# Performance work log

Measured on AMD Instinct MI355X. Metric: run time of the kernel, lower is better.

Reference implementation:

```python
import jax, jax.numpy as jnp
import numpy as np

N = 8192          # total nodes (bipartite: first half left, second half right)
E = 65536         # raw edges
D = 256           # emb_dim
H = 8             # heads
HD = D // H       # head_dim = 32
EAD = 2           # edge_attr_dim


def _init(k, shape, fan_in):
    return (jax.random.normal(k, shape, jnp.float32) / np.sqrt(fan_in)).astype(jnp.float32)


def setup_inputs() -> dict:
    key = jax.random.key(0)
    ks = jax.random.split(key, 16)
    x = jax.random.normal(ks[0], (N, D), jnp.float32)
    src = jax.random.randint(ks[1], (E,), 0, N // 2, jnp.int32)
    dst = jax.random.randint(ks[2], (E,), N // 2, N, jnp.int32)
    edge_index = jnp.stack([src, dst])                       # [2, E]
    edge_attr = jax.random.uniform(ks[3], (E, EAD), jnp.float32)
    query_mask = jax.random.randint(ks[4], (E,), 0, 2, jnp.int32).astype(bool)
    return {
        "x": x,
        "edge_index": edge_index,
        "edge_attr": edge_attr,
        "query_mask": query_mask,
        "start_right": N // 2,
        "W_kqv": _init(ks[5], (D, 3 * D), D), "b_kqv": jnp.zeros((3 * D,), jnp.float32),
        "W_edge": _init(ks[6], (EAD, D), EAD), "b_edge": jnp.zeros((D,), jnp.float32),
        "W_att1": _init(ks[7], (3 * HD, HD), 3 * HD), "b_att1": jnp.zeros((HD,), jnp.float32),
        "W_att2": _init(ks[8], (HD, 1), HD), "b_att2": jnp.zeros((1,), jnp.float32),
        "W_out": _init(ks[9], (D, D), D), "b_out": jnp.zeros((D,), jnp.float32),
        "bn_gamma": jnp.ones((D,), jnp.float32), "bn_beta": jnp.zeros((D,), jnp.float32),
    }


def _build_graph(edge_index, query_mask, n):
    """Replicates MetaGNN.forward edge preprocessing (static, int-only)."""
    ei = np.asarray(edge_index)
    qm = np.asarray(query_mask).astype(bool)
    sup = np.where(~qm)[0]                                   # support edges
    # cat([edge_index[:, support], edge_index.flip(0)], dim=1)
    src = np.concatenate([ei[0, sup], ei[1]])
    dst = np.concatenate([ei[1, sup], ei[0]])
    attr_idx = np.concatenate([sup, np.arange(ei.shape[1])])
    # remove_self_loops
    keep = src != dst
    src, dst, attr_idx = src[keep], dst[keep], attr_idx[keep]
    # add_self_loops with fill_value [0, 0]
    loops = np.arange(n)
    src = np.concatenate([src, loops])
    dst = np.concatenate([dst, loops])
    return jnp.asarray(src), jnp.asarray(dst), jnp.asarray(attr_idx)


def _layer(x, src, dst, ea, W_kqv, b_kqv, W_edge, b_edge, W_att1, b_att1,
           W_att2, b_att2, W_out, b_out, bn_gamma, bn_beta):
    n = x.shape[0]
    kqv = x @ W_kqv + b_kqv                                  # [N, 3D]
    q = kqv[dst, :D].reshape(-1, H, HD)                      # x_i (target)
    k = kqv[src, D:2 * D].reshape(-1, H, HD) / np.sqrt(HD)   # x_j (source)
    v = kqv[src, 2 * D:].reshape(-1, H, HD)
    ef = jax.nn.relu((ea @ W_edge + b_edge).reshape(-1, H, HD))
    feat = jnp.concatenate([k, q, ef], axis=-1)              # [E, H, 3*HD]
    hdn = jax.nn.relu(jnp.einsum('ehf,fd->ehd', feat, W_att1) + b_att1)
    logits = (jnp.einsum('ehd,do->eho', hdn, W_att2) + b_att2)[..., 0]  # [E, H]
    # scatter-softmax over destination node segments
    m = jax.ops.segment_max(logits, dst, num_segments=n)
    a = jnp.exp(logits - m[dst])
    s = jax.ops.segment_sum(a, dst, num_segments=n)
    alpha = a / (s[dst] + 1e-16)                             # [E, H]
    msg = (alpha[..., None] * v).reshape(-1, D) @ W_out + b_out
    out = jax.ops.segment_sum(msg, dst, num_segments=n) + x  # aggr='add' + residual
    # BatchNorm1d (training-mode batch statistics, eps=1e-5)
    mu = out.mean(axis=0)
    var = out.var(axis=0)
    return (out - mu) / jnp.sqrt(var + 1e-5) * bn_gamma + bn_beta


def reference(x, edge_index, edge_attr, query_mask, start_right,
              W_kqv, b_kqv, W_edge, b_edge, W_att1, b_att1, W_att2, b_att2,
              W_out, b_out, bn_gamma, bn_beta):
    n = x.shape[0]
    src, dst, attr_idx = _build_graph(edge_index, query_mask, n)
    ea = jnp.concatenate(
        [edge_attr[attr_idx], jnp.zeros((n, edge_attr.shape[1]), edge_attr.dtype)], axis=0)
    return _layer(x, src, dst, ea, W_kqv, b_kqv, W_edge, b_edge,
                  W_att1, b_att1, W_att2, b_att2, W_out, b_out, bn_gamma, bn_beta)
```

## Files before the change

### kernel.cpp

```cpp
#include <hip/hip_runtime.h>

#define N_NODES 8192
#define E_RAW   65536
#define NSLOT   (2*E_RAW + N_NODES)
#define DEGCAP  64

typedef __attribute__((ext_vector_type(8))) short bf16x8;
typedef __attribute__((ext_vector_type(4))) short bf16x4;
typedef __attribute__((ext_vector_type(4))) float f32x4;
typedef unsigned short u16;

__device__ __forceinline__ u16 f2b(float f) {
  unsigned u = __float_as_uint(f);
  u = (u + 0x7FFFu + ((u >> 16) & 1u)) >> 16;
  return (u16)u;
}
__device__ __forceinline__ float b2f(u16 b) {
  return __uint_as_float(((unsigned)b) << 16);
}

__global__ __launch_bounds__(256) void setup_k(
    const float* __restrict__ x, u16* __restrict__ xb,
    const float* __restrict__ W_kqv, const float* __restrict__ b_kqv,
    const float* __restrict__ W_att1, const float* __restrict__ b_att1,
    const float* __restrict__ W_out,
    u16* __restrict__ BcatT, float* __restrict__ biascat,
    u16* __restrict__ wa1t, u16* __restrict__ WoutT,
    const int* __restrict__ ei, const int* __restrict__ qm,
    const float* __restrict__ eattr,
    int* __restrict__ cnt, int* __restrict__ esrc2, float2* __restrict__ ea2)
{
  __shared__ float tile[64][65];
  const float inv_sqrt_hd = 0.17677669529663687f;
  int bx = blockIdx.x, t = threadIdx.x;

  if (bx < 2048) {
    int i = bx * 256 + t;
    float4 v = ((const float4*)x)[i];
    ushort4 o;
    o.x = f2b(v.x); o.y = f2b(v.y); o.z = f2b(v.z); o.w = f2b(v.w);
    ((ushort4*)xb)[i] = o;
    return;
  }
  if (bx < 2836) {
    int c = bx - 2048;
    int i = t;
    if (c < 768) {
      float v;
      if (c < 256) {
        int h = c >> 5, d2 = c & 31;
        float s = 0.f;
        #pragma unroll
        for (int j = 0; j < 32; ++j)
          s += W_kqv[i*768 + 256 + h*32 + j] * W_att1[j*32 + d2];
        v = s * inv_sqrt_hd;
      } else if (c < 512) {
        int c2 = c - 256; int h = c2 >> 5, d2 = c2 & 31;
        float s = 0.f;
        #pragma unroll
        for (int j = 0; j < 32; ++j)
          s += W_kqv[i*768 + h*32 + j] * W_att1[(32+j)*32 + d2];
        v = s;
      } else {
        v = W_kqv[i*768 + c];
      }
      BcatT[(size_t)c * 256 + i] = f2b(v);
      if (i == 0) {
        float bv;
        if (c < 256) {
          int h = c >> 5, d2 = c & 31;
          float s = 0.f;
          for (int j = 0; j < 32; ++j)
            s += b_kqv[256 + h*32 + j] * W_att1[j*32 + d2];
          bv = s * inv_sqrt_hd;
        } else if (c < 512) {
          int c2 = c - 256; int h = c2 >> 5, d2 = c2 & 31;
          float s = 0.f;
          for (int j = 0; j < 32; ++j)
            s += b_kqv[h*32 + j] * W_att1[(32+j)*32 + d2];
          bv = s + b_att1[c2 & 31];
        } else {
          bv = b_kqv[c];
        }
        biascat[c] = bv;
      }
    } else if (c < 772) {
      int idx = (c - 768) * 256 + i;
      int d2 = idx >> 5, j = idx & 31;
      wa1t[idx] = f2b(W_att1[(64 + j) * 32 + d2]);
    } else {
      int b = c - 772;
      int r0 = (b >> 2) * 64, c0 = (b & 3) * 64;
      for (int idx = i; idx < 4096; idx += 256) {
        int r = idx >> 6, cc = idx & 63;
        tile[r][cc] = W_out[(size_t)(r0 + r) * 256 + c0 + cc];
      }
      __syncthreads();
      for (int idx = i; idx < 4096; idx += 256) {
        int cc = idx >> 6, r = idx & 63;
        WoutT[(size_t)(c0 + cc) * 256 + r0 + r] = f2b(tile[r][cc]);
      }
    }
    return;
  }
  int slot = (bx - 2836) * 256 + t;
  if (slot >= NSLOT) return;
  int src, dst; float a0 = 0.f, a1 = 0.f;
  if (slot < E_RAW) {
    if (qm[slot] != 0) return;
    src = ei[slot]; dst = ei[E_RAW + slot];
    a0 = eattr[2*slot]; a1 = eattr[2*slot + 1];
  } else if (slot < 2*E_RAW) {
    int e = slot - E_RAW;
    src = ei[E_RAW + e]; dst = ei[e];
    a0 = eattr[2*e]; a1 = eattr[2*e + 1];
  } else {
    int n = slot - 2*E_RAW;
    src = n; dst = n;
  }
  int pos = atomicAdd(&cnt[dst], 1);
  if (pos < DEGCAP) {
    esrc2[dst*DEGCAP + pos] = src;
    ea2[dst*DEGCAP + pos] = make_float2(a0, a1);
  }
}

__global__ __launch_bounds__(256) void gemm_nf_k(const u16* __restrict__ xb,
                                                 const u16* __restrict__ BcatT,
                                                 const float* __restrict__ biascat,
                                                 u16* __restrict__ nodeF) {
  int t = threadIdx.x, lane = t & 63, wid = t >> 6;
  int r0 = (blockIdx.x * 4 + wid) * 32;
  int c0 = blockIdx.y * 32;
  int lr = lane & 15, lk = (lane >> 4) * 8;
  f32x4 acc00 = {0.f,0.f,0.f,0.f}, acc01 = {0.f,0.f,0.f,0.f};
  f32x4 acc10 = {0.f,0.f,0.f,0.f}, acc11 = {0.f,0.f,0.f,0.f};
  for (int k0 = 0; k0 < 256; k0 += 32) {
    bf16x8 a0 = *(const bf16x8*)&xb[(size_t)(r0 + lr) * 256 + k0 + lk];
    bf16x8 a1 = *(const bf16x8*)&xb[(size_t)(r0 + 16 + lr) * 256 + k0 + lk];
    bf16x8 b0 = *(const bf16x8*)&BcatT[(size_t)(c0 + lr) * 256 + k0 + lk];
    bf16x8 b1 = *(const bf16x8*)&BcatT[(size_t)(c0 + 16 + lr) * 256 + k0 + lk];
    acc00 = __builtin_amdgcn_mfma_f32_16x16x32_bf16(a0, b0, acc00, 0, 0, 0);
    acc01 = __builtin_amdgcn_mfma_f32_16x16x32_bf16(a0, b1, acc01, 0, 0, 0);
    acc10 = __builtin_amdgcn_mfma_f32_16x16x32_bf16(a1, b0, acc10, 0, 0, 0);
    acc11 = __builtin_amdgcn_mfma_f32_16x16x32_bf16(a1, b1, acc11, 0, 0, 0);
  }
  float bias0 = biascat[c0 + lr];
  float bias1 = biascat[c0 + 16 + lr];
  int rbase = r0 + (lane >> 4) * 4;
  #pragma unroll
  for (int r = 0; r < 4; ++r) {
    nodeF[(size_t)(rbase + r) * 768 + c0 + lr]           = f2b(acc00[r] + bias0);
    nodeF[(size_t)(rbase + r) * 768 + c0 + 16 + lr]      = f2b(acc01[r] + bias1);
    nodeF[(size_t)(rbase + 16 + r) * 768 + c0 + lr]      = f2b(acc10[r] + bias0);
    nodeF[(size_t)(rbase + 16 + r) * 768 + c0 + 16 + lr] = f2b(acc11[r] + bias1);
  }
}

__global__ __launch_bounds__(256) void attn_k(
    const int* __restrict__ cnt, const int* __restrict__ esrc2,
    const float2* __restrict__ ea2, const u16* __restrict__ nf,
    const u16* __restrict__ wa1t,
    const float* __restrict__ W_edge, const float* __restrict__ b_edge,
    const float* __restrict__ W_att2,
    u16* __restrict__ aggb)
{
  __shared__ u16   kws[4][2*336];
  __shared__ float lgs[4][DEGCAP*8];

  int t = threadIdx.x, lane = t & 63, wid = t >> 6;
  int n = blockIdx.x * 4 + wid;
  int deg = cnt[n]; if (deg > DEGCAP) deg = DEGCAP;

  int my_src = 0; float2 my_ea = make_float2(0.f, 0.f);
  if (lane < deg) {
    my_src = esrc2[n * DEGCAP + lane];
    my_ea  = ea2[n * DEGCAP + lane];
  }

  int h_a = lane & 7, j0 = (lane >> 4) * 8;
  float4 w0a = *(const float4*)&W_edge[h_a*32 + j0];
  float4 w0b = *(const float4*)&W_edge[h_a*32 + j0 + 4];
  float4 w1a = *(const float4*)&W_edge[256 + h_a*32 + j0];
  float4 w1b = *(const float4*)&W_edge[256 + h_a*32 + j0 + 4];
  float4 bba = *(const float4*)&b_edge[h_a*32 + j0];
  float4 bbb = *(const float4*)&b_edge[h_a*32 + j0 + 4];
  bf16x8 b0 = *(const bf16x8*)&wa1t[(lane & 15) * 32 + j0];
  bf16x8 b1 = *(const bf16x8*)&wa1t[512 + (lane & 15) * 32 + j0];
  float w2a = W_att2[lane & 15], w2b = W_att2[16 + (lane & 15)];
  int eoff = (lane >> 3) & 1;
  int d2 = lane & 15;

  float qwr0[4], qwr1[4];
  #pragma unroll
  for (int r = 0; r < 4; ++r) {
    int hh = ((lane >> 4) * 4 + r) & 7;
    qwr0[r] = b2f(nf[(size_t)n * 768 + 256 + hh * 32 + d2]);
    qwr1[r] = b2f(nf[(size_t)n * 768 + 256 + hh * 32 + 16 + d2]);
  }

  int el = lane >> 5, kl = lane & 31;
  int hw = kl >> 2, kw_ = kl & 3;

  int ee = el; if (ee >= deg) ee = deg - 1;
  int s_pf = __shfl(my_src, ee);
  bf16x8 kv_pf = *(const bf16x8*)&nf[(size_t)s_pf * 768 + kl * 8];

  for (int e0 = 0; e0 < deg; e0 += 2) {
    bf16x8 kv_cur = kv_pf;
    if (e0 + 2 < deg) {
      int en = e0 + 2 + el; if (en >= deg) en = deg - 1;
      int sn = __shfl(my_src, en);
      kv_pf = *(const bf16x8*)&nf[(size_t)sn * 768 + kl * 8];
    }
    int eaE = e0 + eoff; if (eaE >= deg) eaE = deg - 1;
    float a0 = __shfl(my_ea.x, eaE), a1 = __shfl(my_ea.y, eaE);
    bf16x8 af;
    { float v;
      v = fmaf(a0, w0a.x, fmaf(a1, w1a.x, bba.x)); af[0] = (short)f2b(fmaxf(v, 0.f));
      v = fmaf(a0, w0a.y, fmaf(a1, w1a.y, bba.y)); af[1] = (short)f2b(fmaxf(v, 0.f));
      v = fmaf(a0, w0a.z, fmaf(a1, w1a.z, bba.z)); af[2] = (short)f2b(fmaxf(v, 0.f));
      v = fmaf(a0, w0a.w, fmaf(a1, w1a.w, bba.w)); af[3] = (short)f2b(fmaxf(v, 0.f));
      v = fmaf(a0, w0b.x, fmaf(a1, w1b.x, bbb.x)); af[4] = (short)f2b(fmaxf(v, 0.f));
      v = fmaf(a0, w0b.y, fmaf(a1, w1b.y, bbb.y)); af[5] = (short)f2b(fmaxf(v, 0.f));
      v = fmaf(a0, w0b.z, fmaf(a1, w1b.z, bbb.z)); af[6] = (short)f2b(fmaxf(v, 0.f));
      v = fmaf(a0, w0b.w, fmaf(a1, w1b.w, bbb.w)); af[7] = (short)f2b(fmaxf(v, 0.f));
    }
    *(bf16x8*)&kws[wid][el * 336 + hw * 40 + kw_ * 8] = kv_cur;
    __builtin_amdgcn_wave_barrier();
    f32x4 acc0 = {0.f,0.f,0.f,0.f}, acc1 = {0.f,0.f,0.f,0.f};
    acc0 = __builtin_amdgcn_mfma_f32_16x16x32_bf16(af, b0, acc0, 0, 0, 0);
    acc1 = __builtin_amdgcn_mfma_f32_16x16x32_bf16(af, b1, acc1, 0, 0, 0);
    #pragma unroll
    for (int r = 0; r < 4; ++r) {
      int grr = (lane >> 4) * 4 + r;
      int e = e0 + (grr >> 3), hh = grr & 7;
      float kv0 = b2f(kws[wid][(grr >> 3) * 336 + hh * 40 + d2]);
      float kv1 = b2f(kws[wid][(grr >> 3) * 336 + hh * 40 + 16 + d2]);
      float p0 = acc0[r] + kv0 + qwr0[r];
      float p1 = acc1[r] + kv1 + qwr1[r];
      float vv = fmaxf(p0, 0.f) * w2a + fmaxf(p1, 0.f) * w2b;
      vv += __shfl_xor(vv, 1); vv += __shfl_xor(vv, 2);
      vv += __shfl_xor(vv, 4); vv += __shfl_xor(vv, 8);
      if (d2 == 0 && e < deg) lgs[wid][e * 8 + hh] = vv;
    }
    __builtin_amdgcn_wave_barrier();
  }

  {
    int hh = lane & 7;
    float m = -3.4e38f, s = 0.f;
    for (int i = lane >> 3; i < deg; i += 8) {
      float val = lgs[wid][i * 8 + hh];
      float mn = fmaxf(m, val);
      s = s * __expf(m - mn) + __expf(val - mn);
      m = mn;
    }
    #pragma unroll
    for (int msk = 8; msk <= 32; msk <<= 1) {
      float mo = __shfl_xor(m, msk), so = __shfl_xor(s, msk);
      float mn = fmaxf(m, mo);
      s = s * __expf(m - mn) + so * __expf(mo - mn);
      m = mn;
    }
    float sinv = 1.f / (s + 1e-16f);
    for (int idx = lane; idx < deg * 8; idx += 64)
      lgs[wid][idx] = __expf(lgs[wid][idx] - m) * sinv;
  }
  __builtin_amdgcn_wave_barrier();

  {
    float ac0 = 0.f, ac1 = 0.f, ac2 = 0.f, ac3 = 0.f;
    int head = lane >> 3;
    const u16* vb = nf + 512 + lane * 4;
    #pragma unroll 4
    for (int i = 0; i < deg; ++i) {
      float a = lgs[wid][i * 8 + head];
      int s = __shfl(my_src, i);
      bf16x4 v = *(const bf16x4*)&vb[(size_t)s * 768];
      ac0 = fmaf(a, b2f((u16)v[0]), ac0);
      ac1 = fmaf(a, b2f((u16)v[1]), ac1);
      ac2 = fmaf(a, b2f((u16)v[2]), ac2);
      ac3 = fmaf(a, b2f((u16)v[3]), ac3);
    }
    ushort4 o; o.x = f2b(ac0); o.y = f2b(ac1); o.z = f2b(ac2); o.w = f2b(ac3);
    *(ushort4*)&aggb[(size_t)n * 256 + lane * 4] = o;
  }
}

__global__ __launch_bounds__(256) void gemmout_k(const u16* __restrict__ aggb,
                                                 const u16* __restrict__ WoutT,
                                                 const float* __restrict__ x,
                                                 const int* __restrict__ cnt,
                                                 const float* __restrict__ b_out,
                                                 float* __restrict__ out,
                                                 float* __restrict__ bnsum,
                                                 float* __restrict__ bnsq) {
  int t = threadIdx.x, lane = t & 63, wid = t >> 6;
  int r0 = (blockIdx.x * 4 + wid) * 32;
  int c0 = blockIdx.y * 32;
  int lr = lane & 15, lk = (lane >> 4) * 8;
  f32x4 acc00 = {0.f,0.f,0.f,0.f}, acc01 = {0.f,0.f,0.f,0.f};
  f32x4 acc10 = {0.f,0.f,0.f,0.f}, acc11 = {0.f,0.f,0.f,0.f};
  for (int k0 = 0; k0 < 256; k0 += 32) {
    bf16x8 a0 = *(const bf16x8*)&aggb[(size_t)(r0 + lr) * 256 + k0 + lk];
    bf16x8 a1 = *(const bf16x8*)&aggb[(size_t)(r0 + 16 + lr) * 256 + k0 + lk];
    bf16x8 b0 = *(const bf16x8*)&WoutT[(size_t)(c0 + lr) * 256 + k0 + lk];
    bf16x8 b1 = *(const bf16x8*)&WoutT[(size_t)(c0 + 16 + lr) * 256 + k0 + lk];
    acc00 = __builtin_amdgcn_mfma_f32_16x16x32_bf16(a0, b0, acc00, 0, 0, 0);
    acc01 = __builtin_amdgcn_mfma_f32_16x16x32_bf16(a0, b1, acc01, 0, 0, 0);
    acc10 = __builtin_amdgcn_mfma_f32_16x16x32_bf16(a1, b0, acc10, 0, 0, 0);
    acc11 = __builtin_amdgcn_mfma_f32_16x16x32_bf16(a1, b1, acc11, 0, 0, 0);
  }
  int colA = c0 + lr, colB = c0 + 16 + lr;
  float bA = b_out[colA], bB = b_out[colB];
  int rbase = r0 + (lane >> 4) * 4;
  float sA = 0.f, qA = 0.f, sB = 0.f, qB = 0.f;
  #pragma unroll
  for (int r = 0; r < 4; ++r) {
    int rowA = rbase + r, rowB = rbase + 16 + r;
    float degA = (float)cnt[rowA], degB = (float)cnt[rowB];
    float v00 = acc00[r] + x[(size_t)rowA * 256 + colA] + degA * bA;
    float v01 = acc01[r] + x[(size_t)rowA * 256 + colB] + degA * bB;
    float v10 = acc10[r] + x[(size_t)rowB * 256 + colA] + degB * bA;
    float v11 = acc11[r] + x[(size_t)rowB * 256 + colB] + degB * bB;
    out[(size_t)rowA * 256 + colA] = v00;
    out[(size_t)rowA * 256 + colB] = v01;
    out[(size_t)rowB * 256 + colA] = v10;
    out[(size_t)rowB * 256 + colB] = v11;
    sA += v00 + v10; qA += v00*v00 + v10*v10;
    sB += v01 + v11; qB += v01*v01 + v11*v11;
  }
  #pragma unroll
  for (int msk = 16; msk <= 32; msk <<= 1) {
    sA += __shfl_xor(sA, msk); qA += __shfl_xor(qA, msk);
    sB += __shfl_xor(sB, msk); qB += __shfl_xor(qB, msk);
  }
  if (lane < 16) {
    atomicAdd(&bnsum[colA], sA); atomicAdd(&bnsq[colA], qA);
    atomicAdd(&bnsum[colB], sB); atomicAdd(&bnsq[colB], qB);
  }
}

__global__ __launch_bounds__(256) void bnapply_k(float* __restrict__ out,
                                                 const float* __restrict__ bnsum,
                                                 const float* __restrict__ bnsq,
                                                 const float* __restrict__ gamma,
                                                 const float* __restrict__ beta) {
  int t = threadIdx.x;
  int r = blockIdx.x;
  float mu = bnsum[t] * (1.f / 8192.f);
  float var = bnsq[t] * (1.f / 8192.f) - mu*mu;
  float inv = rsqrtf(var + 1e-5f);
  size_t idx = (size_t)r*256 + t;
  out[idx] = (out[idx] - mu) * inv * gamma[t] + beta[t];
}

extern "C" void kernel_launch(void* const* d_in, const int* in_sizes, int n_in,
                              void* d_out, int out_size, void* d_ws, size_t ws_size,
                              hipStream_t stream) {
  (void)in_sizes; (void)n_in; (void)out_size; (void)ws_size;
  const float* x      = (const float*)d_in[0];
  const int*   ei     = (const int*)d_in[1];
  const float* eattr  = (const float*)d_in[2];
  const int*   qm     = (const int*)d_in[3];
  const float* W_kqv  = (const float*)d_in[5];
  const float* b_kqv  = (const float*)d_in[6];
  const float* W_edge = (const float*)d_in[7];
  const float* b_edge = (const float*)d_in[8];
  const float* W_att1 = (const float*)d_in[9];
  const float* b_att1 = (const float*)d_in[10];
  const float* W_att2 = (const float*)d_in[11];
  const float* W_out  = (const float*)d_in[13];
  const float* b_out  = (const float*)d_in[14];
  const float* gamma  = (const float*)d_in[15];
  const float* beta   = (const float*)d_in[16];
  float* out = (float*)d_out;

  char* w = (char*)d_ws;
  u16*    xb      = (u16*)w;     w += (size_t)N_NODES*256*2;
  u16*    BcatT   = (u16*)w;     w += (size_t)768*256*2;
  u16*    wa1t    = (u16*)w;     w += 1024*2;
  u16*    WoutT   = (u16*)w;     w += (size_t)256*256*2;
  u16*    nodeFb  = (u16*)w;     w += (size_t)N_NODES*768*2;
  float*  biascat = (float*)w;   w += 768*4;
  u16*    aggb    = (u16*)w;     w += (size_t)N_NODES*256*2;
  int*    cnt     = (int*)w;     w += N_NODES*4;
  float*  bnsum   = (float*)w;   w += 256*4;
  float*  bnsq    = (float*)w;   w += 256*4;
  int*    esrc2   = (int*)w;     w += (size_t)N_NODES*DEGCAP*4;
  float2* ea2     = (float2*)w;  w += (size_t)N_NODES*DEGCAP*8;

  hipMemsetAsync(cnt, 0, (size_t)(N_NODES + 512) * sizeof(int), stream);

  setup_k<<<3380, 256, 0, stream>>>(x, xb, W_kqv, b_kqv, W_att1, b_att1, W_out,
                                    BcatT, biascat, wa1t, WoutT,
                                    ei, qm, eattr, cnt, esrc2, ea2);

  gemm_nf_k<<<dim3(N_NODES/128, 768/32), 256, 0, stream>>>(xb, BcatT, biascat, nodeFb);

  attn_k<<<N_NODES/4, 256, 0, stream>>>(cnt, esrc2, ea2, nodeFb, wa1t,
                                        W_edge, b_edge, W_att2, aggb);

  gemmout_k<<<dim3(N_NODES/128, 256/32), 256, 0, stream>>>(
      aggb, WoutT, x, cnt, b_out, out, bnsum, bnsq);

  bnapply_k<<<N_NODES, 256, 0, stream>>>(out, bnsum, bnsq, gamma, beta);
}
```

Before: 116.2 us.

## Split attention into edge-parallel logits kernel and node-parallel aggregation kernel

Moves edge bucketing out of setup and into a new edge-parallel kernel that computes attention logits for each edge, reading its own source/destination rows, and writes them into per-destination CSR slots. A separate node-parallel kernel then does the segment softmax and value aggregation from the stored logits. The aim is to balance work across edges instead of per-node waves with uneven degree, and to drop the per-node sequential logit loop. The cost is an extra round-trip of logits through global memory and one more kernel launch. DEGCAP also drops from 64 to 48, which risks truncating high-degree nodes.

New measurement: 143.8 us. 1.24x slower.

```diff
diff --git a/kernel.cpp b/kernel.cpp
--- a/kernel.cpp
+++ b/kernel.cpp
@@ -3,7 +3,8 @@
 #define N_NODES 8192
 #define E_RAW   65536
 #define NSLOT   (2*E_RAW + N_NODES)
-#define DEGCAP  64
+#define DEGCAP  48
+#define LITER   2
 
 typedef __attribute__((ext_vector_type(8))) short bf16x8;
 typedef __attribute__((ext_vector_type(4))) short bf16x4;
@@ -25,10 +26,7 @@
     const float* __restrict__ W_att1, const float* __restrict__ b_att1,
     const float* __restrict__ W_out,
     u16* __restrict__ BcatT, float* __restrict__ biascat,
-    u16* __restrict__ wa1t, u16* __restrict__ WoutT,
-    const int* __restrict__ ei, const int* __restrict__ qm,
-    const float* __restrict__ eattr,
-    int* __restrict__ cnt, int* __restrict__ esrc2, float2* __restrict__ ea2)
+    u16* __restrict__ wa1t, u16* __restrict__ WoutT)
 {
   __shared__ float tile[64][65];
   const float inv_sqrt_hd = 0.17677669529663687f;
@@ -42,86 +40,63 @@
     ((ushort4*)xb)[i] = o;
     return;
   }
-  if (bx < 2836) {
-    int c = bx - 2048;
-    int i = t;
-    if (c < 768) {
-      float v;
+  int c = bx - 2048;
+  int i = t;
+  if (c < 768) {
+    float v;
+    if (c < 256) {
+      int h = c >> 5, d2 = c & 31;
+      float s = 0.f;
+      #pragma unroll
+      for (int j = 0; j < 32; ++j)
+        s += W_kqv[i*768 + 256 + h*32 + j] * W_att1[j*32 + d2];
+      v = s * inv_sqrt_hd;
+    } else if (c < 512) {
+      int c2 = c - 256; int h = c2 >> 5, d2 = c2 & 31;
+      float s = 0.f;
+      #pragma unroll
+      for (int j = 0; j < 32; ++j)
+        s += W_kqv[i*768 + h*32 + j] * W_att1[(32+j)*32 + d2];
+      v = s;
+    } else {
+      v = W_kqv[i*768 + c];
+    }
+    BcatT[(size_t)c * 256 + i] = f2b(v);
+    if (i == 0) {
+      float bv;
       if (c < 256) {
         int h = c >> 5, d2 = c & 31;
         float s = 0.f;
-        #pragma unroll
         for (int j = 0; j < 32; ++j)
-          s += W_kqv[i*768 + 256 + h*32 + j] * W_att1[j*32 + d2];
-        v = s * inv_sqrt_hd;
+          s += b_kqv[256 + h*32 + j] * W_att1[j*32 + d2];
+        bv = s * inv_sqrt_hd;
       } else if (c < 512) {
         int c2 = c - 256; int h = c2 >> 5, d2 = c2 & 31;
         float s = 0.f;
-        #pragma unroll
         for (int j = 0; j < 32; ++j)
-          s += W_kqv[i*768 + h*32 + j] * W_att1[(32+j)*32 + d2];
-        v = s;
+          s += b_kqv[h*32 + j] * W_att1[(32+j)*32 + d2];
+        bv = s + b_att1[c2 & 31];
       } else {
-        v = W_kqv[i*768 + c];
+        bv = b_kqv[c];
       }
-      BcatT[(size_t)c * 256 + i] = f2b(v);
-      if (i == 0) {
-        float bv;
-        if (c < 256) {
-          int h = c >> 5, d2 = c & 31;
-          float s = 0.f;
-          for (int j = 0; j < 32; ++j)
-            s += b_kqv[256 + h*32 + j] * W_att1[j*32 + d2];
-          bv = s * inv_sqrt_hd;
-        } else if (c < 512) {
-          int c2 = c - 256; int h = c2 >> 5, d2 = c2 & 31;
-          float s = 0.f;
-          for (int j = 0; j < 32; ++j)
-            s += b_kqv[h*32 + j] * W_att1[(32+j)*32 + d2];
-          bv = s + b_att1[c2 & 31];
-        } else {
-          bv = b_kqv[c];
-        }
-        biascat[c] = bv;
-      }
-    } else if (c < 772) {
-      int idx = (c - 768) * 256 + i;
-      int d2 = idx >> 5, j = idx & 31;
-      wa1t[idx] = f2b(W_att1[(64 + j) * 32 + d2]);
-    } else {
-      int b = c - 772;
-      int r0 = (b >> 2) * 64, c0 = (b & 3) * 64;
-      for (int idx = i; idx < 4096; idx += 256) {
-        int r = idx >> 6, cc = idx & 63;
-        tile[r][cc] = W_out[(size_t)(r0 + r) * 256 + c0 + cc];
-      }
-      __syncthreads();
-      for (int idx = i; idx < 4096; idx += 256) {
-        int cc = idx >> 6, r = idx & 63;
-        WoutT[(size_t)(c0 + cc) * 256 + r0 + r] = f2b(tile[r][cc]);
-      }
-    }
-    return;
-  }
-  int slot = (bx - 2836) * 256 + t;
-  if (slot >= NSLOT) return;
-  int src, dst; float a0 = 0.f, a1 = 0.f;
-  if (slot < E_RAW) {
-    if (qm[slot] != 0) return;
-    src = ei[slot]; dst = ei[E_RAW + slot];
-    a0 = eattr[2*slot]; a1 = eattr[2*slot + 1];
-  } else if (slot < 2*E_RAW) {
-    int e = slot - E_RAW;
-    src = ei[E_RAW + e]; dst = ei[e];
-    a0 = eattr[2*e]; a1 = eattr[2*e + 1];
+      biascat[c] = bv;
+    }
+  } else if (c < 772) {
+    int idx = (c - 768) * 256 + i;
+    int d2 = idx >> 5, j = idx & 31;
+    wa1t[idx] = f2b(W_att1[(64 + j) * 32 + d2]);
   } else {
-    int n = slot - 2*E_RAW;
-    src = n; dst = n;
-  }
-  int pos = atomicAdd(&cnt[dst], 1);
-  if (pos < DEGCAP) {
-    esrc2[dst*DEGCAP + pos] = src;
-    ea2[dst*DEGCAP + pos] = make_float2(a0, a1);
+    int b = c - 772;
+    int r0 = (b >> 2) * 64, c0 = (b & 3) * 64;
+    for (int idx = i; idx < 4096; idx += 256) {
+      int r = idx >> 6, cc = idx & 63;
+      tile[r][cc] = W_out[(size_t)(r0 + r) * 256 + c0 + cc];
+    }
+    __syncthreads();
+    for (int idx = i; idx < 4096; idx += 256) {
+      int cc = idx >> 6, r = idx & 63;
+      WoutT[(size_t)(c0 + cc) * 256 + r0 + r] = f2b(tile[r][cc]);
+    }
   }
 }
 
@@ -157,26 +132,17 @@
   }
 }
 
-__global__ __launch_bounds__(256) void attn_k(
-    const int* __restrict__ cnt, const int* __restrict__ esrc2,
-    const float2* __restrict__ ea2, const u16* __restrict__ nf,
+__global__ __launch_bounds__(256) void logits_k(
+    const int* __restrict__ ei, const int* __restrict__ qm,
+    const float* __restrict__ eattr, const u16* __restrict__ nf,
     const u16* __restrict__ wa1t,
     const float* __restrict__ W_edge, const float* __restrict__ b_edge,
     const float* __restrict__ W_att2,
-    u16* __restrict__ aggb)
+    int* __restrict__ cnt, int* __restrict__ src_csr, float* __restrict__ lg)
 {
-  __shared__ u16   kws[4][2*336];
-  __shared__ float lgs[4][DEGCAP*8];
+  __shared__ __align__(16) u16 kq[4][4][336];
 
   int t = threadIdx.x, lane = t & 63, wid = t >> 6;
-  int n = blockIdx.x * 4 + wid;
-  int deg = cnt[n]; if (deg > DEGCAP) deg = DEGCAP;
-
-  int my_src = 0; float2 my_ea = make_float2(0.f, 0.f);
-  if (lane < deg) {
-    my_src = esrc2[n * DEGCAP + lane];
-    my_ea  = ea2[n * DEGCAP + lane];
-  }
 
   int h_a = lane & 7, j0 = (lane >> 4) * 8;
   float4 w0a = *(const float4*)&W_edge[h_a*32 + j0];
@@ -188,33 +154,46 @@
   bf16x8 b0 = *(const bf16x8*)&wa1t[(lane & 15) * 32 + j0];
   bf16x8 b1 = *(const bf16x8*)&wa1t[512 + (lane & 15) * 32 + j0];
   float w2a = W_att2[lane & 15], w2b = W_att2[16 + (lane & 15)];
-  int eoff = (lane >> 3) & 1;
   int d2 = lane & 15;
-
-  float qwr0[4], qwr1[4];
-  #pragma unroll
-  for (int r = 0; r < 4; ++r) {
-    int hh = ((lane >> 4) * 4 + r) & 7;
-    qwr0[r] = b2f(nf[(size_t)n * 768 + 256 + hh * 32 + d2]);
-    qwr1[r] = b2f(nf[(size_t)n * 768 + 256 + hh * 32 + 16 + d2]);
-  }
-
-  int el = lane >> 5, kl = lane & 31;
-  int hw = kl >> 2, kw_ = kl & 3;
-
-  int ee = el; if (ee >= deg) ee = deg - 1;
-  int s_pf = __shfl(my_src, ee);
-  bf16x8 kv_pf = *(const bf16x8*)&nf[(size_t)s_pf * 768 + kl * 8];
-
-  for (int e0 = 0; e0 < deg; e0 += 2) {
-    bf16x8 kv_cur = kv_pf;
-    if (e0 + 2 < deg) {
-      int en = e0 + 2 + el; if (en >= deg) en = deg - 1;
-      int sn = __shfl(my_src, en);
-      kv_pf = *(const bf16x8*)&nf[(size_t)sn * 768 + kl * 8];
-    }
-    int eaE = e0 + eoff; if (eaE >= deg) eaE = deg - 1;
-    float a0 = __shfl(my_ea.x, eaE), a1 = __shfl(my_ea.y, eaE);
+  int rslot = lane >> 4, re = rslot & 1, rtype = rslot >> 1;
+
+  for (int it = 0; it < LITER; ++it) {
+    int s0 = (blockIdx.x * LITER + it) * 8 + wid * 2;
+
+    int slot = s0 + re;
+    int src, dst, validL = 1;
+    if (slot < E_RAW) {
+      validL = (qm[slot] == 0);
+      src = ei[slot]; dst = ei[E_RAW + slot];
+    } else if (slot < 2*E_RAW) {
+      int e = slot - E_RAW;
+      src = ei[E_RAW + e]; dst = ei[e];
+    } else {
+      int nn = slot - 2*E_RAW;
+      src = nn; dst = nn;
+    }
+
+    int node = rtype ? dst : src;
+    const u16* rp = &nf[(size_t)node * 768 + (rtype ? 256 : 0) + (lane & 15) * 16];
+    bf16x8 rv0 = *(const bf16x8*)rp;
+    bf16x8 rv1 = *(const bf16x8*)(rp + 8);
+
+    int valid0 = __shfl(validL, 0),  valid1 = __shfl(validL, 16);
+    int dst0   = __shfl(dst, 32),    dst1   = __shfl(dst, 48);
+    int src0v  = __shfl(src, 0),     src1v  = __shfl(src, 16);
+
+    int myPos = 0;
+    if (lane == 0 && valid0) myPos = atomicAdd(&cnt[dst0], 1);
+    if (lane == 1 && valid1) myPos = atomicAdd(&cnt[dst1], 1);
+    int pos0 = __shfl(myPos, 0), pos1 = __shfl(myPos, 1);
+
+    int slot_ea = s0 + ((lane >> 3) & 1);
+    float a0 = 0.f, a1 = 0.f;
+    if (slot_ea < 2*E_RAW) {
+      int em = slot_ea < E_RAW ? slot_ea : slot_ea - E_RAW;
+      float2 ld = *(const float2*)&eattr[2*em];
+      a0 = ld.x; a1 = ld.y;
+    }
     bf16x8 af;
     { float v;
       v = fmaf(a0, w0a.x, fmaf(a1, w1a.x, bba.x)); af[0] = (short)f2b(fmaxf(v, 0.f));
@@ -226,66 +205,96 @@
       v = fmaf(a0, w0b.z, fmaf(a1, w1b.z, bbb.z)); af[6] = (short)f2b(fmaxf(v, 0.f));
       v = fmaf(a0, w0b.w, fmaf(a1, w1b.w, bbb.w)); af[7] = (short)f2b(fmaxf(v, 0.f));
     }
-    *(bf16x8*)&kws[wid][el * 336 + hw * 40 + kw_ * 8] = kv_cur;
+
+    {
+      int idx0 = (lane & 15) * 2;
+      *(bf16x8*)&kq[wid][rslot][(idx0 >> 2) * 40 + (idx0 & 3) * 8] = rv0;
+      int idx1 = idx0 + 1;
+      *(bf16x8*)&kq[wid][rslot][(idx1 >> 2) * 40 + (idx1 & 3) * 8] = rv1;
+    }
     __builtin_amdgcn_wave_barrier();
+
     f32x4 acc0 = {0.f,0.f,0.f,0.f}, acc1 = {0.f,0.f,0.f,0.f};
     acc0 = __builtin_amdgcn_mfma_f32_16x16x32_bf16(af, b0, acc0, 0, 0, 0);
     acc1 = __builtin_amdgcn_mfma_f32_16x16x32_bf16(af, b1, acc1, 0, 0, 0);
+
+    float vvs[4];
     #pragma unroll
     for (int r = 0; r < 4; ++r) {
       int grr = (lane >> 4) * 4 + r;
-      int e = e0 + (grr >> 3), hh = grr & 7;
-      float kv0 = b2f(kws[wid][(grr >> 3) * 336 + hh * 40 + d2]);
-      float kv1 = b2f(kws[wid][(grr >> 3) * 336 + hh * 40 + 16 + d2]);
-      float p0 = acc0[r] + kv0 + qwr0[r];
-      float p1 = acc1[r] + kv1 + qwr1[r];
+      int e = grr >> 3, hh = grr & 7;
+      float kv0 = b2f(kq[wid][e][hh * 40 + d2]);
+      float kv1 = b2f(kq[wid][e][hh * 40 + 16 + d2]);
+      float qv0 = b2f(kq[wid][2 + e][hh * 40 + d2]);
+      float qv1 = b2f(kq[wid][2 + e][hh * 40 + 16 + d2]);
+      float p0 = acc0[r] + kv0 + qv0;
+      float p1 = acc1[r] + kv1 + qv1;
       float vv = fmaxf(p0, 0.f) * w2a + fmaxf(p1, 0.f) * w2b;
       vv += __shfl_xor(vv, 1); vv += __shfl_xor(vv, 2);
       vv += __shfl_xor(vv, 4); vv += __shfl_xor(vv, 8);
-      if (d2 == 0 && e < deg) lgs[wid][e * 8 + hh] = vv;
+      vvs[r] = vv;
+    }
+
+    if (lane == 0 && valid0 && pos0 < DEGCAP) src_csr[dst0 * DEGCAP + pos0] = src0v;
+    if (lane == 1 && valid1 && pos1 < DEGCAP) src_csr[dst1 * DEGCAP + pos1] = src1v;
+    if (d2 == 0) {
+      #pragma unroll
+      for (int r = 0; r < 4; ++r) {
+        int grr = (lane >> 4) * 4 + r;
+        int e = grr >> 3, hh = grr & 7;
+        int vd = e ? valid1 : valid0;
+        int pp = e ? pos1 : pos0;
+        int dd = e ? dst1 : dst0;
+        if (vd && pp < DEGCAP)
+          lg[((size_t)dd * DEGCAP + pp) * 8 + hh] = vvs[r];
+      }
     }
     __builtin_amdgcn_wave_barrier();
   }
-
-  {
-    int hh = lane & 7;
-    float m = -3.4e38f, s = 0.f;
-    for (int i = lane >> 3; i < deg; i += 8) {
-      float val = lgs[wid][i * 8 + hh];
-      float mn = fmaxf(m, val);
-      s = s * __expf(m - mn) + __expf(val - mn);
-      m = mn;
-    }
-    #pragma unroll
-    for (int msk = 8; msk <= 32; msk <<= 1) {
-      float mo = __shfl_xor(m, msk), so = __shfl_xor(s, msk);
-      float mn = fmaxf(m, mo);
-      s = s * __expf(m - mn) + so * __expf(mo - mn);
-      m = mn;
-    }
-    float sinv = 1.f / (s + 1e-16f);
-    for (int idx = lane; idx < deg * 8; idx += 64)
-      lgs[wid][idx] = __expf(lgs[wid][idx] - m) * sinv;
-  }
-  __builtin_amdgcn_wave_barrier();
-
-  {
-    float ac0 = 0.f, ac1 = 0.f, ac2 = 0.f, ac3 = 0.f;
-    int head = lane >> 3;
-    const u16* vb = nf + 512 + lane * 4;
-    #pragma unroll 4
-    for (int i = 0; i < deg; ++i) {
-      float a = lgs[wid][i * 8 + head];
-      int s = __shfl(my_src, i);
-      bf16x4 v = *(const bf16x4*)&vb[(size_t)s * 768];
-      ac0 = fmaf(a, b2f((u16)v[0]), ac0);
-      ac1 = fmaf(a, b2f((u16)v[1]), ac1);
-      ac2 = fmaf(a, b2f((u16)v[2]), ac2);
-      ac3 = fmaf(a, b2f((u16)v[3]), ac3);
-    }
-    ushort4 o; o.x = f2b(ac0); o.y = f2b(ac1); o.z = f2b(ac2); o.w = f2b(ac3);
-    *(ushort4*)&aggb[(size_t)n * 256 + lane * 4] = o;
-  }
+}
+
+__global__ __launch_bounds__(256) void aggr_k(const int* __restrict__ cnt,
+                                              const int* __restrict__ src_csr,
+                                              const float* __restrict__ lg,
+                                              const u16* __restrict__ nf,
+                                              u16* __restrict__ aggb) {
+  int t = threadIdx.x, lane = t & 63, wid = t >> 6;
+  int n = blockIdx.x * 4 + wid;
+  int deg = cnt[n]; if (deg > DEGCAP) deg = DEGCAP;
+  const float* lgn = lg + (size_t)n * DEGCAP * 8;
+
+  float m = -3.4e38f, s = 0.f;
+  for (int i = lane >> 3; i < deg; i += 8) {
+    float val = lgn[i * 8 + (lane & 7)];
+    float mn = fmaxf(m, val);
+    s = s * __expf(m - mn) + __expf(val - mn);
+    m = mn;
+  }
+  #pragma unroll
+  for (int msk = 8; msk <= 32; msk <<= 1) {
+    float mo = __shfl_xor(m, msk), so = __shfl_xor(s, msk);
+    float mn = fmaxf(m, mo);
+    s = s * __expf(m - mn) + so * __expf(mo - mn);
+    m = mn;
+  }
+  float sinv = 1.f / (s + 1e-16f);
+  int head = lane >> 3;
+  float mh = __shfl(m, head);
+  float sh = __shfl(sinv, head);
+
+  float ac0 = 0.f, ac1 = 0.f, ac2 = 0.f, ac3 = 0.f;
+  const u16* vb = nf + 512 + lane * 4;
+  for (int i = 0; i < deg; ++i) {
+    int srcv = src_csr[n * DEGCAP + i];
+    float a = __expf(lgn[i * 8 + head] - mh) * sh;
+    bf16x4 v = *(const bf16x4*)&vb[(size_t)srcv * 768];
+    ac0 = fmaf(a, b2f((u16)v[0]), ac0);
+    ac1 = fmaf(a, b2f((u16)v[1]), ac1);
+    ac2 = fmaf(a, b2f((u16)v[2]), ac2);
+    ac3 = fmaf(a, b2f((u16)v[3]), ac3);
+  }
+  ushort4 o; o.x = f2b(ac0); o.y = f2b(ac1); o.z = f2b(ac2); o.w = f2b(ac3);
+  *(ushort4*)&aggb[(size_t)n * 256 + lane * 4] = o;
 }
 
 __global__ __launch_bounds__(256) void gemmout_k(const u16* __restrict__ aggb,
@@ -388,19 +397,21 @@
   int*    cnt     = (int*)w;     w += N_NODES*4;
   float*  bnsum   = (float*)w;   w += 256*4;
   float*  bnsq    = (float*)w;   w += 256*4;
-  int*    esrc2   = (int*)w;     w += (size_t)N_NODES*DEGCAP*4;
-  float2* ea2     = (float2*)w;  w += (size_t)N_NODES*DEGCAP*8;
+  int*    src_csr = (int*)w;     w += (size_t)N_NODES*DEGCAP*4;
+  float*  lg      = (float*)w;   w += (size_t)N_NODES*DEGCAP*8*4;
 
   hipMemsetAsync(cnt, 0, (size_t)(N_NODES + 512) * sizeof(int), stream);
 
-  setup_k<<<3380, 256, 0, stream>>>(x, xb, W_kqv, b_kqv, W_att1, b_att1, W_out,
-                                    BcatT, biascat, wa1t, WoutT,
-                                    ei, qm, eattr, cnt, esrc2, ea2);
+  setup_k<<<2836, 256, 0, stream>>>(x, xb, W_kqv, b_kqv, W_att1, b_att1, W_out,
+                                    BcatT, biascat, wa1t, WoutT);
 
   gemm_nf_k<<<dim3(N_NODES/128, 768/32), 256, 0, stream>>>(xb, BcatT, biascat, nodeFb);
 
-  attn_k<<<N_NODES/4, 256, 0, stream>>>(cnt, esrc2, ea2, nodeFb, wa1t,
-                                        W_edge, b_edge, W_att2, aggb);
+  logits_k<<<NSLOT/(8*LITER), 256, 0, stream>>>(ei, qm, eattr, nodeFb, wa1t,
+                                                W_edge, b_edge, W_att2,
+                                                cnt, src_csr, lg);
+
+  aggr_k<<<N_NODES/4, 256, 0, stream>>>(cnt, src_csr, lg, nodeFb, aggb);
 
   gemmout_k<<<dim3(N_NODES/128, 256/32), 256, 0, stream>>>(
       aggb, WoutT, x, cnt, b_out, out, bnsum, bnsq);
```
